# Kernel tuning notes

Measured on AMD Instinct MI355X. Metric: run time of the kernel, lower is better.

Reference implementation:

```python
import jax, jax.numpy as jnp
import numpy as np

SCALE = 1.0  # module scale=1; dropout_p=0 so dropout is identity; selector is Identity


def setup_inputs() -> dict:
    key = jax.random.key(0)
    k0, k1, k2, k3, k4 = jax.random.split(key, 5)
    B, S, DIN, DOUT, P, R = 4, 2048, 4096, 4096, 5, 8
    x = jax.random.normal(k0, (B, S, DIN), dtype=jnp.float32)
    W = jax.random.normal(k1, (DOUT, DIN), dtype=jnp.float32) * 0.02   # nn.Linear weight [out, in]
    lora_down = jax.random.normal(k2, (P, DIN, R), dtype=jnp.float32) * 0.02
    lora_up = jax.random.normal(k3, (P, R, DOUT), dtype=jnp.float32) * 0.02
    lora_route = jax.random.normal(k4, (P, DIN, P), dtype=jnp.float32) * 0.02
    return {"x": x, "W": W, "lora_down": lora_down, "lora_up": lora_up,
            "lora_route": lora_route, "task_id": 4}


def reference(x, W, lora_down, lora_up, lora_route, task_id):
    tid = task_id  # Python int (static), tid > 1 branch
    # Routing: logits over the first (tid-1) experts using route table of task tid
    logits = jnp.einsum('bsi,ij->bsj', x, lora_route[tid - 1, :, :tid - 1])  # [B,S,tid-1]
    omegas = jax.nn.softmax(logits, axis=-1)
    # Previous experts: (lora_down[j] @ lora_up[j]).detach() -> stop_gradient.
    # Keep low-rank structure: z = x @ down  [B,S,J,R], then weight and project up.
    down_prev = jax.lax.stop_gradient(lora_down[:tid - 1])  # [J, DIN, R]
    up_prev = jax.lax.stop_gradient(lora_up[:tid - 1])      # [J, R, DOUT]
    z = jnp.einsum('bsi,jir->bsjr', x, down_prev)           # [B,S,J,R] small (R=8)
    delta_prev = jnp.einsum('bsjr,jro->bso', z * omegas[..., None], up_prev)
    # Current expert (j == tid-1): live params, no gating weight
    cur = (x @ lora_down[tid - 1]) @ lora_up[tid - 1]       # [B,S,DOUT]
    delta = SCALE * (delta_prev + cur)
    return x @ W.T + delta
```

## Files before the change

kernel.cpp:

```cpp
#include <hip/hip_runtime.h>
#include <hip/hip_bf16.h>

typedef unsigned short u16;
typedef __attribute__((ext_vector_type(8))) __bf16 bf16x8;
typedef __attribute__((ext_vector_type(4))) float f32x4;

#define DIN 4096
#define DOUT 4096
#define MROWS 8192

__device__ __forceinline__ u16 f2bf(float f) {
  unsigned int u = __float_as_uint(f);
  u += 0x7fffu + ((u >> 16) & 1u);
  return (u16)(u >> 16);
}

__device__ __forceinline__ void gl2lds16(const void* g, void* l) {
  __builtin_amdgcn_global_load_lds(
      (const __attribute__((address_space(1))) unsigned int*)g,
      (__attribute__((address_space(3))) unsigned int*)l, 16, 0, 0);
}


__global__ __launch_bounds__(256) void convx(const float* __restrict__ x,
                                             u16* __restrict__ Xb) {
  size_t i = ((size_t)blockIdx.x * 256 + threadIdx.x) * 4;
  float4 v = *(const float4*)(x + i);
  ushort4 o;
  o.x = f2bf(v.x); o.y = f2bf(v.y); o.z = f2bf(v.z); o.w = f2bf(v.w);
  *(ushort4*)(Xb + i) = o;
}

__global__ __launch_bounds__(256) void convw(const float* __restrict__ W,
                                             u16* __restrict__ Wb) {
  size_t i = ((size_t)blockIdx.x * 256 + threadIdx.x) * 4;
  float4 v = *(const float4*)(W + i);
  ushort4 o;
  o.x = f2bf(v.x); o.y = f2bf(v.y); o.z = f2bf(v.z); o.w = f2bf(v.w);
  *(ushort4*)(Wb + i) = o;
}

__global__ __launch_bounds__(256) void convu(const float* __restrict__ up,
                                             u16* __restrict__ Ub) {
  int n = blockIdx.x * 256 + threadIdx.x;
  union { u16 us[32]; uint4 q[4]; } o;
  #pragma unroll
  for (int c = 0; c < 32; ++c) o.us[c] = f2bf(up[(size_t)c * DOUT + n]);
  uint4* dst = (uint4*)(Ub + (size_t)n * 32);
  #pragma unroll
  for (int q = 0; q < 4; ++q) dst[q] = o.q[q];
}

__global__ __launch_bounds__(256) void wtprep(const float* __restrict__ route,
                                              const float* __restrict__ down,
                                              u16* __restrict__ Wt) {
  const int c = blockIdx.y;
  const int k0 = blockIdx.x * 1024 + threadIdx.x * 4;
  const float* route3 = route + 3 * DIN * 5;
  float v[4];
  #pragma unroll
  for (int j = 0; j < 4; ++j) {
    int k = k0 + j;
    float f;
    if (c < 3)       f = route3[(size_t)k * 5 + c];
    else if (c < 35) f = down[(size_t)((c - 3) >> 3) * DIN * 8 + (size_t)k * 8 + ((c - 3) & 7)];
    else             f = 0.f;
    v[j] = f;
  }
  ushort4 o;
  o.x = f2bf(v[0]); o.y = f2bf(v[1]); o.z = f2bf(v[2]); o.w = f2bf(v[3]);
  *(ushort4*)(Wt + (size_t)c * DIN + k0) = o;
}

__global__ __launch_bounds__(256) void coeffgemm(
    const u16* __restrict__ Xb, const u16* __restrict__ Wt,
    float* __restrict__ Pw) {
  __shared__ __align__(16) u16 As[128 * 64];
  __shared__ __align__(16) u16 Bs[48 * 64];
  const int tid = threadIdx.x;
  const int m0 = blockIdx.x * 128;
  const int kb = blockIdx.y * 512;
  const int lane = tid & 63;
  const int w = tid >> 6;
  const int wr = w * 32;
  const int fm = lane & 15;
  const int xr = fm & 7;
  const int qd = lane >> 4;

  f32x4 acc[2][3];
  #pragma unroll
  for (int i = 0; i < 2; ++i)
    #pragma unroll
    for (int j = 0; j < 3; ++j) acc[i][j] = (f32x4){0.f, 0.f, 0.f, 0.f};

  const int srow = tid >> 3;
  const int scol = ((tid & 7) ^ (srow & 7)) * 8;
  const u16* gA = Xb + (size_t)(m0 + srow) * DIN + kb + scol;
  u16* lA = As + tid * 8;

  for (int kc = 0; kc < 512; kc += 64) {
    gl2lds16(Wt + (size_t)srow * DIN + kb + kc + scol, Bs + tid * 8);
    if (tid < 128) {
      int u = 256 + tid;
      int usw = ((u & 7) ^ ((u >> 3) & 7)) * 8;
      gl2lds16(Wt + (size_t)(u >> 3) * DIN + kb + kc + usw, Bs + u * 8);
    }
    #pragma unroll
    for (int it = 0; it < 4; ++it)
      gl2lds16(gA + kc + (size_t)(it * 32) * DIN, lA + it * 2048);
    __syncthreads();
    #pragma unroll
    for (int kk = 0; kk < 64; kk += 32) {
      const int q = (kk >> 3) + qd;
      bf16x8 af[2], bfr[3];
      #pragma unroll
      for (int i = 0; i < 2; ++i)
        af[i] = *(const bf16x8*)(As + (wr + i * 16 + fm) * 64 + ((q ^ xr) << 3));
      #pragma unroll
      for (int j = 0; j < 3; ++j)
        bfr[j] = *(const bf16x8*)(Bs + (j * 16 + fm) * 64 + ((q ^ xr) << 3));
      #pragma unroll
      for (int i = 0; i < 2; ++i)
        #pragma unroll
        for (int j = 0; j < 3; ++j)
          acc[i][j] = __builtin_amdgcn_mfma_f32_16x16x32_bf16(af[i], bfr[j], acc[i][j], 0, 0, 0);
    }
    __syncthreads();
  }
  const int em = (lane >> 4) * 4;
  const int en = lane & 15;
  const size_t pbase = (size_t)blockIdx.y * MROWS;
  #pragma unroll
  for (int i = 0; i < 2; ++i)
    #pragma unroll
    for (int j = 0; j < 3; ++j)
      #pragma unroll
      for (int r = 0; r < 4; ++r)
        Pw[(pbase + m0 + wr + i * 16 + em + r) * 48 + j * 16 + en] = acc[i][j][r];
}

__global__ __launch_bounds__(256) void reduce_coeff(const float* __restrict__ Pw,
                                                    u16* __restrict__ Cb) {
  const int tid = threadIdx.x;
  const int rl = tid >> 2;
  const int cg = tid & 3;
  const int m = blockIdx.x * 64 + rl;
  const int lane = tid & 63;

  float s[12];
  #pragma unroll
  for (int q = 0; q < 12; ++q) s[q] = 0.f;
  for (int sp = 0; sp < 8; ++sp) {
    const float4* p = (const float4*)(Pw + ((size_t)sp * MROWS + m) * 48 + cg * 12);
    #pragma unroll
    for (int q = 0; q < 3; ++q) {
      float4 v = p[q];
      s[q * 4 + 0] += v.x; s[q * 4 + 1] += v.y;
      s[q * 4 + 2] += v.z; s[q * 4 + 3] += v.w;
    }
  }
  const int src = lane & ~3;
  const float L0 = __shfl(s[0], src);
  const float L1 = __shfl(s[1], src);
  const float L2 = __shfl(s[2], src);
  const float mx = fmaxf(L0, fmaxf(L1, L2));
  const float e0 = __expf(L0 - mx), e1 = __expf(L1 - mx), e2 = __expf(L2 - mx);
  const float inv = 1.f / (e0 + e1 + e2);
  const float om0 = e0 * inv, om1 = e1 * inv, om2 = e2 * inv;
  #pragma unroll
  for (int j = 0; j < 12; ++j) {
    const int G = cg * 12 + j;
    if (G >= 3 && G < 35) {
      const float wgt = (G < 11) ? om0 : (G < 19) ? om1 : (G < 27) ? om2 : 1.f;
      Cb[(size_t)m * 32 + (G - 3)] = f2bf(s[j] * wgt);
    }
  }
}


#define MF(a, b, c) __builtin_amdgcn_mfma_f32_16x16x32_bf16(a, b, c, 0, 0, 0)

#define MROW(A, I) \
  acc[I][0] = MF(A, bfr0, acc[I][0]); \
  acc[I][1] = MF(A, bfr1, acc[I][1]); \
  acc[I][2] = MF(A, bfr2, acc[I][2]); \
  acc[I][3] = MF(A, bfr3, acc[I][3]);

#define VM4 asm volatile("s_waitcnt vmcnt(4)" ::: "memory")
#define VM0 asm volatile("s_waitcnt vmcnt(0)" ::: "memory")

#define STA(REG, KOFF) { const u16* s_ = gA + (KOFF); \
  gl2lds16(s_, dA + (REG) * 8192); \
  gl2lds16(s_ + 128 * 4096, dA + (REG) * 8192 + 4096); }
#define STB(REG, KOFF) { const u16* s_ = gB + (KOFF); \
  gl2lds16(s_, dB + (REG) * 8192); \
  gl2lds16(s_ + 128 * 4096, dB + (REG) * 8192 + 4096); }
#define STC { const u16* s_ = Cb + (size_t)(m0 + gr1) * 32 + kc1; \
  gl2lds16(s_, dA); gl2lds16(s_ + 128 * 32, dA + 4096); }
#define STU { const u16* s_ = Ub + (size_t)(n0 + gr1) * 32 + kc1; \
  gl2lds16(s_, dB); gl2lds16(s_ + 128 * 32, dB + 4096); }

#define PH(REG, IH, LOADB, ISSUE, VMX) { \
  const u16* ap_ = sm + (REG) * 8192 + wmoff + (IH) * 2048 + off0; \
  bf16x8 af0 = *(const bf16x8*)(ap_); \
  bf16x8 af1 = *(const bf16x8*)(ap_ + 512); \
  bf16x8 af2 = *(const bf16x8*)(ap_ + 1024); \
  bf16x8 af3 = *(const bf16x8*)(ap_ + 1536); \
  if (LOADB) { \
    const u16* bp_ = sm + 32768 + (REG) * 8192 + wnoff + off0; \
    bfr0 = *(const bf16x8*)(bp_); \
    bfr1 = *(const bf16x8*)(bp_ + 512); \
    bfr2 = *(const bf16x8*)(bp_ + 1024); \
    bfr3 = *(const bf16x8*)(bp_ + 1536); \
  } \
  ISSUE; \
  asm volatile("" ::: "memory"); \
  __builtin_amdgcn_s_barrier(); \
  __builtin_amdgcn_s_setprio(1); \
  MROW(af0, (IH) * 4 + 0) \
  MROW(af1, (IH) * 4 + 1) \
  MROW(af2, (IH) * 4 + 2) \
  MROW(af3, (IH) * 4 + 3) \
  __builtin_amdgcn_s_setprio(0); \
  VMX; \
  asm volatile("" ::: "memory"); \
  __builtin_amdgcn_s_barrier(); \
}

#define TILE(B, I1, I2, I3, I4, VMX) { \
  bf16x8 bfr0, bfr1, bfr2, bfr3; \
  PH((B) * 2 + 0, 0, 1, I1, (void)0) \
  PH((B) * 2 + 0, 1, 0, I2, (void)0) \
  PH((B) * 2 + 1, 0, 1, I3, (void)0) \
  PH((B) * 2 + 1, 1, 0, I4, VMX) \
}

__global__ __launch_bounds__(512, 2) void gemm_fused8(
    const u16* __restrict__ Xb, const u16* __restrict__ Wb,
    const u16* __restrict__ Cb, const u16* __restrict__ Ub,
    float* __restrict__ out) {
  __shared__ __align__(16) u16 sm[65536];
  const int tid = threadIdx.x;
  const int bid = blockIdx.x;
  const int wg = (bid & 7) * 64 + (bid >> 3);
  const int mt = wg >> 4;
  const int nt = wg & 15;
  const int m0 = mt * 256;
  const int n0 = nt * 256;
  const int lane = tid & 63;
  const int w = tid >> 6;
  const int wm = w >> 2;
  const int wn = w & 3;
  const int fm = lane & 15;
  const int qd = lane >> 4;
  const int off0 = (fm >> 1) * 64 + (((((fm & 1) << 2) | qd)) ^ (fm >> 1)) * 8;
  const int wmoff = wm * 4096;
  const int wnoff = wn * 2048;

  const int c1 = (tid & 7) ^ ((tid >> 3) & 7);
  const int gr1 = 2 * (tid >> 3) + (c1 >> 2);
  const int kc1 = (c1 & 3) * 8;
  const u16* gA = Xb + (size_t)(m0 + gr1) * 4096 + kc1;
  const u16* gB = Wb + (size_t)(n0 + gr1) * 4096 + kc1;
  u16* dA = sm + tid * 8;
  u16* dB = sm + 32768 + tid * 8;

  f32x4 acc[8][4];
  #pragma unroll
  for (int i = 0; i < 8; ++i)
    #pragma unroll
    for (int j = 0; j < 4; ++j) acc[i][j] = (f32x4){0.f, 0.f, 0.f, 0.f};

  STA(0, 0)  STB(0, 0)
  STA(1, 32) STB(1, 32)
  STA(2, 64) STB(2, 64)
  VM4;
  asm volatile("" ::: "memory");
  __builtin_amdgcn_s_barrier();

  for (int T = 0; T < 62; T += 2) {
    TILE(0, STA(3, T * 64 + 96),  STB(3, T * 64 + 96),
            STA(0, T * 64 + 128), STB(0, T * 64 + 128), VM4)
    TILE(1, STA(1, T * 64 + 160), STB(1, T * 64 + 160),
            STA(2, T * 64 + 192), STB(2, T * 64 + 192), VM4)
  }
  TILE(0, STA(3, 4064), STB(3, 4064), (void)0, (void)0, VM0)
  TILE(1, STC, STU, (void)0, (void)0, VM0)

  {
    const u16* ap = sm + wmoff + off0;
    const u16* bp = sm + 32768 + wnoff + off0;
    bf16x8 bfr0 = *(const bf16x8*)(bp);
    bf16x8 bfr1 = *(const bf16x8*)(bp + 512);
    bf16x8 bfr2 = *(const bf16x8*)(bp + 1024);
    bf16x8 bfr3 = *(const bf16x8*)(bp + 1536);
    #pragma unroll
    for (int i = 0; i < 8; ++i) {
      bf16x8 a = *(const bf16x8*)(ap + i * 512);
      acc[i][0] = MF(a, bfr0, acc[i][0]);
      acc[i][1] = MF(a, bfr1, acc[i][1]);
      acc[i][2] = MF(a, bfr2, acc[i][2]);
      acc[i][3] = MF(a, bfr3, acc[i][3]);
    }
  }

  const int em = qd * 4;
  const int en = fm;
  const size_t obase = (size_t)(m0 + wm * 128) * DOUT + n0 + wn * 64 + en;
  #pragma unroll
  for (int i = 0; i < 8; ++i)
    #pragma unroll
    for (int j = 0; j < 4; ++j)
      #pragma unroll
      for (int r = 0; r < 4; ++r)
        out[obase + (size_t)(i * 16 + em + r) * DOUT + j * 16] = acc[i][j][r];
}

extern "C" void kernel_launch(void* const* d_in, const int* in_sizes, int n_in,
                              void* d_out, int out_size, void* d_ws, size_t ws_size,
                              hipStream_t stream) {
  const float* x     = (const float*)d_in[0];
  const float* W     = (const float*)d_in[1];
  const float* down  = (const float*)d_in[2];
  const float* up    = (const float*)d_in[3];
  const float* route = (const float*)d_in[4];
  float* out = (float*)d_out;

  char* ws = (char*)d_ws;
  u16*   Xb = (u16*)ws;
  u16*   Wb = (u16*)(ws + 67108864);
  u16*   Cb = (u16*)(ws + 100663296);
  u16*   Ub = (u16*)(ws + 101187584);
  u16*   Wt = (u16*)(ws + 101449728);
  float* Pw = (float*)(ws + 101842944);

  convx<<<32768, 256, 0, stream>>>(x, Xb);
  convw<<<16384, 256, 0, stream>>>(W, Wb);
  convu<<<16, 256, 0, stream>>>(up, Ub);
  wtprep<<<dim3(4, 48), 256, 0, stream>>>(route, down, Wt);
  coeffgemm<<<dim3(64, 8), 256, 0, stream>>>(Xb, Wt, Pw);
  reduce_coeff<<<128, 256, 0, stream>>>(Pw, Cb);
  gemm_fused8<<<512, 512, 0, stream>>>(Xb, Wb, Cb, Ub, out);
}
```

Baseline: 510.2 us.

## Double-buffer LDS fragments in registers and halve barriers per GEMM phase

```diff
diff --git a/kernel.cpp b/kernel.cpp
--- a/kernel.cpp
+++ b/kernel.cpp
@@ -180,11 +180,11 @@
 
 #define MF(a, b, c) __builtin_amdgcn_mfma_f32_16x16x32_bf16(a, b, c, 0, 0, 0)
 
-#define MROW(A, I) \
-  acc[I][0] = MF(A, bfr0, acc[I][0]); \
-  acc[I][1] = MF(A, bfr1, acc[I][1]); \
-  acc[I][2] = MF(A, bfr2, acc[I][2]); \
-  acc[I][3] = MF(A, bfr3, acc[I][3]);
+#define MROW2(IH, I, BA, BB) \
+  acc[(IH)*4+(I)][0] = MF(fA[BA][I], fB[BB][0], acc[(IH)*4+(I)][0]); \
+  acc[(IH)*4+(I)][1] = MF(fA[BA][I], fB[BB][1], acc[(IH)*4+(I)][1]); \
+  acc[(IH)*4+(I)][2] = MF(fA[BA][I], fB[BB][2], acc[(IH)*4+(I)][2]); \
+  acc[(IH)*4+(I)][3] = MF(fA[BA][I], fB[BB][3], acc[(IH)*4+(I)][3]);
 
 #define VM4 asm volatile("s_waitcnt vmcnt(4)" ::: "memory")
 #define VM0 asm volatile("s_waitcnt vmcnt(0)" ::: "memory")
@@ -200,39 +200,38 @@
 #define STU { const u16* s_ = Ub + (size_t)(n0 + gr1) * 32 + kc1; \
   gl2lds16(s_, dB); gl2lds16(s_ + 128 * 32, dB + 4096); }
 
-#define PH(REG, IH, LOADB, ISSUE, VMX) { \
-  const u16* ap_ = sm + (REG) * 8192 + wmoff + (IH) * 2048 + off0; \
-  bf16x8 af0 = *(const bf16x8*)(ap_); \
-  bf16x8 af1 = *(const bf16x8*)(ap_ + 512); \
-  bf16x8 af2 = *(const bf16x8*)(ap_ + 1024); \
-  bf16x8 af3 = *(const bf16x8*)(ap_ + 1536); \
-  if (LOADB) { \
-    const u16* bp_ = sm + 32768 + (REG) * 8192 + wnoff + off0; \
-    bfr0 = *(const bf16x8*)(bp_); \
-    bfr1 = *(const bf16x8*)(bp_ + 512); \
-    bfr2 = *(const bf16x8*)(bp_ + 1024); \
-    bfr3 = *(const bf16x8*)(bp_ + 1536); \
-  } \
+#define PHW(IH, BA, BB, PFA, NREG, NIH, NBA, PFB, NBB, ISSUE, VMX) { \
   ISSUE; \
   asm volatile("" ::: "memory"); \
   __builtin_amdgcn_s_barrier(); \
-  __builtin_amdgcn_s_setprio(1); \
-  MROW(af0, (IH) * 4 + 0) \
-  MROW(af1, (IH) * 4 + 1) \
-  MROW(af2, (IH) * 4 + 2) \
-  MROW(af3, (IH) * 4 + 3) \
-  __builtin_amdgcn_s_setprio(0); \
+  asm volatile("" ::: "memory"); \
   VMX; \
   asm volatile("" ::: "memory"); \
-  __builtin_amdgcn_s_barrier(); \
-}
-
-#define TILE(B, I1, I2, I3, I4, VMX) { \
-  bf16x8 bfr0, bfr1, bfr2, bfr3; \
-  PH((B) * 2 + 0, 0, 1, I1, (void)0) \
-  PH((B) * 2 + 0, 1, 0, I2, (void)0) \
-  PH((B) * 2 + 1, 0, 1, I3, (void)0) \
-  PH((B) * 2 + 1, 1, 0, I4, VMX) \
+  __builtin_amdgcn_s_setprio(1); \
+  if (PFA) { \
+    const u16* np_ = sm + (NREG) * 8192 + wmoff + (NIH) * 2048 + off0; \
+    fA[NBA][0] = *(const bf16x8*)(np_); \
+    fA[NBA][1] = *(const bf16x8*)(np_ + 512); \
+    fA[NBA][2] = *(const bf16x8*)(np_ + 1024); \
+    fA[NBA][3] = *(const bf16x8*)(np_ + 1536); \
+  } \
+  if (PFB) { \
+    const u16* nb_ = sm + 32768 + (NREG) * 8192 + wnoff + off0; \
+    fB[NBB][0] = *(const bf16x8*)(nb_); \
+    fB[NBB][1] = *(const bf16x8*)(nb_ + 512); \
+    fB[NBB][2] = *(const bf16x8*)(nb_ + 1024); \
+    fB[NBB][3] = *(const bf16x8*)(nb_ + 1536); \
+  } \
+  MROW2(IH, 0, BA, BB) MROW2(IH, 1, BA, BB) \
+  MROW2(IH, 2, BA, BB) MROW2(IH, 3, BA, BB) \
+  __builtin_amdgcn_s_setprio(0); \
+}
+
+#define TILEW(R0, R1, R0N, I1, I2, I3, I4, VMX4) { \
+  PHW(0, 0, 0, 1, R0, 1, 1, 0, 0, I1, (void)0) \
+  PHW(1, 1, 0, 1, R1, 0, 0, 1, 1, I2, (void)0) \
+  PHW(0, 0, 1, 1, R1, 1, 1, 0, 0, I3, (void)0) \
+  PHW(1, 1, 1, 1, R0N, 0, 0, 1, 0, I4, VMX4) \
 }
 
 __global__ __launch_bounds__(512, 2) void gemm_fused8(
@@ -271,21 +270,41 @@
     #pragma unroll
     for (int j = 0; j < 4; ++j) acc[i][j] = (f32x4){0.f, 0.f, 0.f, 0.f};
 
+  bf16x8 fA[2][4];
+  bf16x8 fB[2][4];
+
   STA(0, 0)  STB(0, 0)
   STA(1, 32) STB(1, 32)
   STA(2, 64) STB(2, 64)
   VM4;
   asm volatile("" ::: "memory");
   __builtin_amdgcn_s_barrier();
+  asm volatile("" ::: "memory");
+  {
+    const u16* pp = sm + wmoff + off0;
+    fA[0][0] = *(const bf16x8*)(pp);
+    fA[0][1] = *(const bf16x8*)(pp + 512);
+    fA[0][2] = *(const bf16x8*)(pp + 1024);
+    fA[0][3] = *(const bf16x8*)(pp + 1536);
+    const u16* pb = sm + 32768 + wnoff + off0;
+    fB[0][0] = *(const bf16x8*)(pb);
+    fB[0][1] = *(const bf16x8*)(pb + 512);
+    fB[0][2] = *(const bf16x8*)(pb + 1024);
+    fB[0][3] = *(const bf16x8*)(pb + 1536);
+  }
 
   for (int T = 0; T < 62; T += 2) {
-    TILE(0, STA(3, T * 64 + 96),  STB(3, T * 64 + 96),
-            STA(0, T * 64 + 128), STB(0, T * 64 + 128), VM4)
-    TILE(1, STA(1, T * 64 + 160), STB(1, T * 64 + 160),
-            STA(2, T * 64 + 192), STB(2, T * 64 + 192), VM4)
-  }
-  TILE(0, STA(3, 4064), STB(3, 4064), (void)0, (void)0, VM0)
-  TILE(1, STC, STU, (void)0, (void)0, VM0)
+    TILEW(0, 1, 2, STA(3, T * 64 + 96),  STB(3, T * 64 + 96),
+                   STA(0, T * 64 + 128), STB(0, T * 64 + 128), VM4)
+    TILEW(2, 3, 0, STA(1, T * 64 + 160), STB(1, T * 64 + 160),
+                   STA(2, T * 64 + 192), STB(2, T * 64 + 192), VM4)
+  }
+  TILEW(0, 1, 2, STA(3, 4064), STB(3, 4064), (void)0, (void)0, VM0)
+  TILEW(2, 3, 0, STC, STU, (void)0, (void)0, VM0)
+
+  asm volatile("" ::: "memory");
+  __builtin_amdgcn_s_barrier();
+  asm volatile("" ::: "memory");
 
   {
     const u16* ap = sm + wmoff + off0;
```

After: 502.8 us. Within noise of the previous version (-1.4%).
